# Kernel tuning notes

Hardware: AMD Instinct MI355X
Metric: run time of the kernel (lower is better)

Reference implementation:

```python
import jax, jax.numpy as jnp
import numpy as np
from functools import partial

T, B, IN, H, OUT = 512, 64, 512, 1024, 512


def _qrnn_layer(x, W, b):
    """One QRNN layer (window=1, fo-pool). x: (T,B,D) -> (T,B,H)."""
    g = jnp.einsum('tbd,dh->tbh', x, W) + b        # (T,B,3H)
    z, f, o = jnp.split(g, 3, axis=-1)
    z = jnp.tanh(z)
    f = jax.nn.sigmoid(f)
    o = jax.nn.sigmoid(o)

    def step(c, zf):
        z_t, f_t = zf
        c = f_t * c + (1.0 - f_t) * z_t            # fo-pool recurrence
        return c, c

    c0 = jnp.zeros((x.shape[1], W.shape[1] // 3), x.dtype)
    _, cs = jax.lax.scan(step, c0, (z, f))         # cs: (T,B,H)
    return o * cs


def setup_inputs() -> dict:
    key = jax.random.key(0)
    ks = jax.random.split(key, 5)
    scale = lambda fan_in: 1.0 / np.sqrt(fan_in)
    return {
        'x':   jax.random.normal(ks[0], (T, B, IN), jnp.float32),
        'W0':  jax.random.normal(ks[1], (IN, 3 * H), jnp.float32) * scale(IN),
        'b0':  jnp.zeros((3 * H,), jnp.float32),
        'W1':  jax.random.normal(ks[2], (H, 3 * H), jnp.float32) * scale(H),
        'b1':  jnp.zeros((3 * H,), jnp.float32),
        'Wfc': jax.random.normal(ks[3], (H, OUT), jnp.float32) * scale(H),
        'bfc': jnp.zeros((OUT,), jnp.float32),
    }


def reference(x, W0, b0, W1, b1, Wfc, bfc):
    h = _qrnn_layer(x, W0, b0)                     # layer 0: (T,B,H)
    h = _qrnn_layer(h, W1, b1)                     # layer 1: (T,B,H)
    out = jnp.einsum('tbh,ho->tbo', h, Wfc) + bfc  # fc over all timesteps
    return out
```

## Files before the change

### kernel.cpp

```cpp
#include <hip/hip_runtime.h>
#include <hip/hip_bf16.h>


#define QT 512
#define QB 64
#define QIN 512
#define QH 1024
#define QOUT 512
#define QM (QT * QB)
#define SEG 32
#define SL (QT / SEG)

typedef unsigned short ushort_t;
typedef __attribute__((ext_vector_type(8))) short bf16x8;
typedef __attribute__((ext_vector_type(4))) float f32x4;

__device__ __forceinline__ float u2f(ushort_t u) {
    union { unsigned int i; float f; } v;
    v.i = ((unsigned int)u) << 16;
    return v.f;
}

__device__ __forceinline__ ushort_t f2bf(float f) {
    union { float f; unsigned int i; } v;
    v.f = f;
    unsigned int r = v.i + 0x7fffu + ((v.i >> 16) & 1u);
    return (ushort_t)(r >> 16);
}

__device__ __forceinline__ void glds16(const ushort_t* g, ushort_t* l) {
    __builtin_amdgcn_global_load_lds(
        (const __attribute__((address_space(1))) void*)g,
        (__attribute__((address_space(3))) void*)l, 16, 0, 0);
}

__global__ __launch_bounds__(256) void cvt_bf16(const float* __restrict__ src,
                                                ushort_t* __restrict__ dst) {
    const int i = blockIdx.x * 256 + threadIdx.x;
    float4 v = ((const float4*)src)[i];
    ushort4 o;
    o.x = f2bf(v.x); o.y = f2bf(v.y); o.z = f2bf(v.z); o.w = f2bf(v.w);
    ((ushort4*)dst)[i] = o;
}

__global__ __launch_bounds__(256) void transpose_cvt(
    const float* __restrict__ W, ushort_t* __restrict__ WT, int K, int N) {
    __shared__ float t[32][33];
    const int tx = threadIdx.x & 31, ty = threadIdx.x >> 5;
    const int n0 = blockIdx.x * 32, k0 = blockIdx.y * 32;
#pragma unroll
    for (int i = 0; i < 4; ++i)
        t[ty + 8 * i][tx] = W[(size_t)(k0 + ty + 8 * i) * N + n0 + tx];
    __syncthreads();
#pragma unroll
    for (int i = 0; i < 4; ++i)
        WT[(size_t)(n0 + ty + 8 * i) * K + k0 + tx] = f2bf(t[tx][ty + 8 * i]);
}

template <int MODE, int K>
__global__ __launch_bounds__(512, 2) void gemm256(
    const ushort_t* __restrict__ A, const ushort_t* __restrict__ BT,
    const float* __restrict__ bias, void* __restrict__ out,
    int c0, int CW) {
    constexpr int NT = K / 32;
    __shared__ ushort_t As[4 * 8192];
    __shared__ ushort_t Bs[4 * 8192];

    const int tid = threadIdx.x;
    const int lane = tid & 63;
    const int w = tid >> 6;
    const int wr = w >> 2, wc = w & 3;

    const int gx = gridDim.x;
    const int nwg = gx * gridDim.y;
    int flat = blockIdx.y * gx + blockIdx.x;
    flat = (flat & 7) * (nwg >> 3) + (flat >> 3);
    const int by = flat / gx;
    const int bx = flat - by * gx;
    const int m0 = by * 256;

    int nW, nOut, outstride, gate = 0;
    if (MODE == 0) {
        const int per = CW >> 8;
        gate = bx / per;
        const int nloc = (bx - gate * per) * 256;
        nW = gate * QH + c0 + nloc;
        nOut = gate * CW + nloc;
        outstride = 3 * CW;
    } else {
        nW = bx * 256;
        nOut = nW;
        outstride = QOUT;
    }

    size_t aoff[2], boff[2];
    int ldso[2];
#pragma unroll
    for (int j = 0; j < 2; ++j) {
        const int c = w * 128 + j * 64 + lane;
        const int r = c >> 2;
        const int gs = (c & 3) ^ ((r >> 1) & 3);
        aoff[j] = (size_t)(m0 + r) * K + gs * 8;
        boff[j] = (size_t)(nW + r) * K + gs * 8;
        ldso[j] = w * 1024 + j * 512;
    }

    const int fl = lane & 15, fq = lane >> 4;
    const int laneoff = fl * 32 + ((fq ^ ((fl >> 1) & 3)) << 3);

    f32x4 acc[8][4];
#pragma unroll
    for (int i = 0; i < 8; ++i)
#pragma unroll
        for (int j = 0; j < 4; ++j) acc[i][j] = {0.f, 0.f, 0.f, 0.f};

#pragma unroll
    for (int t = 0; t < 3; ++t) {
        const int slot = t * 8192;
#pragma unroll
        for (int j = 0; j < 2; ++j)
            glds16(A + aoff[j] + t * 32, &As[slot + ldso[j]]);
#pragma unroll
        for (int j = 0; j < 2; ++j)
            glds16(BT + boff[j] + t * 32, &Bs[slot + ldso[j]]);
    }
    asm volatile("s_waitcnt vmcnt(8)" ::: "memory");
    __builtin_amdgcn_s_barrier();

    for (int kt = 0; kt < NT; ++kt) {
        if (kt + 3 < NT) {
            const int slot = ((kt + 3) & 3) * 8192;
            const size_t kb = (size_t)(kt + 3) * 32;
#pragma unroll
            for (int j = 0; j < 2; ++j)
                glds16(A + aoff[j] + kb, &As[slot + ldso[j]]);
#pragma unroll
            for (int j = 0; j < 2; ++j)
                glds16(BT + boff[j] + kb, &Bs[slot + ldso[j]]);
        }
        const int sa = (kt & 3) * 8192 + wr * 4096 + laneoff;
        const int sb = (kt & 3) * 8192 + wc * 2048 + laneoff;
        bf16x8 af[8], bv[4];
#pragma unroll
        for (int i = 0; i < 8; ++i) af[i] = *(const bf16x8*)&As[sa + i * 512];
#pragma unroll
        for (int j = 0; j < 4; ++j) bv[j] = *(const bf16x8*)&Bs[sb + j * 512];
        __builtin_amdgcn_s_setprio(1);
#pragma unroll
        for (int i = 0; i < 8; ++i)
#pragma unroll
            for (int j = 0; j < 4; ++j)
                acc[i][j] = __builtin_amdgcn_mfma_f32_16x16x32_bf16(
                    af[i], bv[j], acc[i][j], 0, 0, 0);
        __builtin_amdgcn_s_setprio(0);
        if (kt < NT - 3)
            asm volatile("s_waitcnt vmcnt(8)" ::: "memory");
        else if (kt == NT - 3)
            asm volatile("s_waitcnt vmcnt(4)" ::: "memory");
        else if (kt == NT - 2)
            asm volatile("s_waitcnt vmcnt(0)" ::: "memory");
        if (kt < NT - 1) __builtin_amdgcn_s_barrier();
    }

    const float ak = (gate == 0) ? 2.8853900817779268f : -1.4426950408889634f;
    const float aa = (gate == 0) ? -2.f : 1.f;
    const float ad = (gate == 0) ? 1.f : 0.f;

#pragma unroll
    for (int j = 0; j < 4; ++j) {
        const int cb = wc * 64 + j * 16 + fl;
        const float bvv = bias[nW + cb];
        const int col = nOut + cb;
#pragma unroll
        for (int i = 0; i < 8; ++i) {
            const int row0 = m0 + wr * 128 + i * 16 + fq * 4;
#pragma unroll
            for (int r = 0; r < 4; ++r) {
                float v = acc[i][j][r] + bvv;
                if (MODE == 0) {
                    v = aa * __builtin_amdgcn_rcpf(
                                 1.f + __builtin_amdgcn_exp2f(ak * v)) +
                        ad;
                    ((ushort_t*)out)[(size_t)(row0 + r) * outstride + col] =
                        f2bf(v);
                } else {
                    ((float*)out)[(size_t)(row0 + r) * outstride + col] = v;
                }
            }
        }
    }
}


__global__ __launch_bounds__(256) void scan_p1(const ushort_t* __restrict__ g,
                                               float* __restrict__ Aseg,
                                               float* __restrict__ Bseg,
                                               int CW) {
    const int idx = blockIdx.x * 256 + threadIdx.x;
    const int hh = idx % CW;
    const int sb = idx / CW;
    const int b = sb % QB;
    const int s = sb / QB;
    const ushort_t* gp = g + ((size_t)(s * SL * QB + b) * 3) * CW + hh;
    const size_t grow = (size_t)QB * 3 * CW;
    float zv[SL], fv[SL];
#pragma unroll
    for (int t = 0; t < SL; ++t) {
        zv[t] = u2f(gp[0]);
        fv[t] = u2f(gp[CW]);
        gp += grow;
    }
    float A = 1.f, Bc = 0.f;
#pragma unroll
    for (int t = 0; t < SL; ++t) {
        Bc = fv[t] * Bc + (1.f - fv[t]) * zv[t];
        A *= fv[t];
    }
    Aseg[idx] = A;
    Bseg[idx] = Bc;
}

__global__ __launch_bounds__(256) void scan_p2(const float* __restrict__ Aseg,
                                               const float* __restrict__ Bseg,
                                               float* __restrict__ cstart,
                                               int CW) {
    const int idx = blockIdx.x * 256 + threadIdx.x;
    const size_t stride = (size_t)QB * CW;
    float Av[SEG], Bv[SEG];
#pragma unroll
    for (int s = 0; s < SEG; ++s) {
        Av[s] = Aseg[s * stride + idx];
        Bv[s] = Bseg[s * stride + idx];
    }
    float c = 0.f;
#pragma unroll
    for (int s = 0; s < SEG; ++s) {
        cstart[s * stride + idx] = c;
        c = Av[s] * c + Bv[s];
    }
}

__global__ __launch_bounds__(256) void scan_p3(const ushort_t* __restrict__ g,
                                               const float* __restrict__ cstart,
                                               ushort_t* __restrict__ h,
                                               int c0, int CW) {
    const int idx = blockIdx.x * 256 + threadIdx.x;
    const int hh = idx % CW;
    const int sb = idx / CW;
    const int b = sb % QB;
    const int s = sb / QB;
    const ushort_t* gp = g + ((size_t)(s * SL * QB + b) * 3) * CW + hh;
    ushort_t* hp = h + (size_t)(s * SL * QB + b) * QH + c0 + hh;
    const size_t grow = (size_t)QB * 3 * CW;
    const size_t hrow = (size_t)QB * QH;
    float zv[SL], fv[SL], ov[SL];
#pragma unroll
    for (int t = 0; t < SL; ++t) {
        zv[t] = u2f(gp[0]);
        fv[t] = u2f(gp[CW]);
        ov[t] = u2f(gp[2 * CW]);
        gp += grow;
    }
    float c = cstart[idx];
#pragma unroll
    for (int t = 0; t < SL; ++t) {
        c = fv[t] * c + (1.f - fv[t]) * zv[t];
        *hp = f2bf(ov[t] * c);
        hp += hrow;
    }
}

extern "C" void kernel_launch(void* const* d_in, const int* in_sizes, int n_in,
                              void* d_out, int out_size, void* d_ws,
                              size_t ws_size, hipStream_t stream) {
    const float* x   = (const float*)d_in[0];
    const float* W0  = (const float*)d_in[1];
    const float* b0  = (const float*)d_in[2];
    const float* W1  = (const float*)d_in[3];
    const float* b1  = (const float*)d_in[4];
    const float* Wfc = (const float*)d_in[5];
    const float* bfc = (const float*)d_in[6];
    float* out = (float*)d_out;

    char* p = (char*)d_ws;
    ushort_t* h0   = (ushort_t*)p;  p += (size_t)QM * QH * 2;
    ushort_t* h1   = (ushort_t*)p;
    ushort_t* x_bf = (ushort_t*)p;  p += (size_t)QM * QH * 2;
    ushort_t* W0T  = (ushort_t*)p;  p += (size_t)3 * QH * QIN * 2;
    ushort_t* W1T  = (ushort_t*)p;  p += (size_t)3 * QH * QH * 2;
    ushort_t* WfcT = (ushort_t*)p;  p += (size_t)QOUT * QH * 2;
    const size_t base = (size_t)(p - (char*)d_ws);

    int CW = QH;
    while (CW > 256 &&
           base + 3 * (size_t)QB * CW * SEG * 4 + (size_t)QM * 3 * CW * 2 >
               ws_size)
        CW >>= 1;
    const int nch = QH / CW;

    float* Aseg   = (float*)p;  p += (size_t)QB * CW * SEG * 4;
    float* Bseg   = (float*)p;  p += (size_t)QB * CW * SEG * 4;
    float* cstart = (float*)p;  p += (size_t)QB * CW * SEG * 4;
    ushort_t* g   = (ushort_t*)p;

    dim3 blk(256);
    dim3 blk5(512);

    cvt_bf16<<<dim3(QM * QIN / 1024), blk, 0, stream>>>(x, x_bf);
    transpose_cvt<<<dim3(3 * QH / 32, QIN / 32), blk, 0, stream>>>(
        W0, W0T, QIN, 3 * QH);
    transpose_cvt<<<dim3(3 * QH / 32, QH / 32), blk, 0, stream>>>(
        W1, W1T, QH, 3 * QH);
    transpose_cvt<<<dim3(QOUT / 32, QH / 32), blk, 0, stream>>>(
        Wfc, WfcT, QH, QOUT);

    const dim3 ggrid(3 * (CW >> 8), QM / 256);
    const dim3 p13grid(SEG * QB * CW / 256);
    const dim3 p2grid(QB * CW / 256);

    for (int ci = 0; ci < nch; ++ci) {
        gemm256<0, QIN><<<ggrid, blk5, 0, stream>>>(x_bf, W0T, b0, g,
                                                    ci * CW, CW);
        scan_p1<<<p13grid, blk, 0, stream>>>(g, Aseg, Bseg, CW);
        scan_p2<<<p2grid, blk, 0, stream>>>(Aseg, Bseg, cstart, CW);
        scan_p3<<<p13grid, blk, 0, stream>>>(g, cstart, h0, ci * CW, CW);
    }
    for (int ci = 0; ci < nch; ++ci) {
        gemm256<0, QH><<<ggrid, blk5, 0, stream>>>(h0, W1T, b1, g,
                                                   ci * CW, CW);
        scan_p1<<<p13grid, blk, 0, stream>>>(g, Aseg, Bseg, CW);
        scan_p2<<<p2grid, blk, 0, stream>>>(Aseg, Bseg, cstart, CW);
        scan_p3<<<p13grid, blk, 0, stream>>>(g, cstart, h1, ci * CW, CW);
    }
    gemm256<1, QH><<<dim3(QOUT / 256, QM / 256), blk5, 0, stream>>>(
        h1, WfcT, bfc, out, 0, 0);
}
```

Before: 786.1 us.

## Split GEMM K-step into two half-tile phases with interleaved LDS reads and prefetch

The main GEMM loop now splits each K-tile into two phases. The first half of the A fragments is loaded and multiplied while the A-tile prefetch is issued, then the second half is loaded alongside the B-tile prefetch. Extra workgroup barriers and sched_barrier fences enforce the ordering so LDS reads, global-to-LDS copies and MFMAs from different waves interleave, and register pressure from fragments drops. The epilogue loop order is also changed to iterate rows outer and columns inner, with bias hoisted. The cost is three extra barriers per K iteration.

```diff
diff --git a/kernel.cpp b/kernel.cpp
--- a/kernel.cpp
+++ b/kernel.cpp
@@ -128,30 +128,56 @@
     __builtin_amdgcn_s_barrier();
 
     for (int kt = 0; kt < NT; ++kt) {
-        if (kt + 3 < NT) {
-            const int slot = ((kt + 3) & 3) * 8192;
-            const size_t kb = (size_t)(kt + 3) * 32;
+        const int slot = (kt & 3) * 8192;
+        const int sa = slot + wr * 4096 + laneoff;
+        const int sb = slot + wc * 2048 + laneoff;
+        const bool pf = (kt + 3 < NT);
+        const int pslot = ((kt + 3) & 3) * 8192;
+        const size_t kb = (size_t)(kt + 3) * 32;
+
+        bf16x8 a0[4], a1[4], bv[4];
+#pragma unroll
+        for (int i = 0; i < 4; ++i) a0[i] = *(const bf16x8*)&As[sa + i * 512];
+#pragma unroll
+        for (int j = 0; j < 4; ++j) bv[j] = *(const bf16x8*)&Bs[sb + j * 512];
+        if (pf) {
 #pragma unroll
             for (int j = 0; j < 2; ++j)
-                glds16(A + aoff[j] + kb, &As[slot + ldso[j]]);
-#pragma unroll
-            for (int j = 0; j < 2; ++j)
-                glds16(BT + boff[j] + kb, &Bs[slot + ldso[j]]);
+                glds16(A + aoff[j] + kb, &As[pslot + ldso[j]]);
         }
-        const int sa = (kt & 3) * 8192 + wr * 4096 + laneoff;
-        const int sb = (kt & 3) * 8192 + wc * 2048 + laneoff;
-        bf16x8 af[8], bv[4];
-#pragma unroll
-        for (int i = 0; i < 8; ++i) af[i] = *(const bf16x8*)&As[sa + i * 512];
-#pragma unroll
-        for (int j = 0; j < 4; ++j) bv[j] = *(const bf16x8*)&Bs[sb + j * 512];
+        __builtin_amdgcn_sched_barrier(0);
+        __builtin_amdgcn_s_barrier();
+        asm volatile("s_waitcnt lgkmcnt(0)" ::: "memory");
+        __builtin_amdgcn_sched_barrier(0);
         __builtin_amdgcn_s_setprio(1);
 #pragma unroll
-        for (int i = 0; i < 8; ++i)
+        for (int i = 0; i < 4; ++i)
 #pragma unroll
             for (int j = 0; j < 4; ++j)
                 acc[i][j] = __builtin_amdgcn_mfma_f32_16x16x32_bf16(
-                    af[i], bv[j], acc[i][j], 0, 0, 0);
+                    a0[i], bv[j], acc[i][j], 0, 0, 0);
+        __builtin_amdgcn_s_setprio(0);
+        __builtin_amdgcn_sched_barrier(0);
+        __builtin_amdgcn_s_barrier();
+#pragma unroll
+        for (int i = 0; i < 4; ++i)
+            a1[i] = *(const bf16x8*)&As[sa + (4 + i) * 512];
+        if (pf) {
+#pragma unroll
+            for (int j = 0; j < 2; ++j)
+                glds16(BT + boff[j] + kb, &Bs[pslot + ldso[j]]);
+        }
+        __builtin_amdgcn_sched_barrier(0);
+        __builtin_amdgcn_s_barrier();
+        asm volatile("s_waitcnt lgkmcnt(0)" ::: "memory");
+        __builtin_amdgcn_sched_barrier(0);
+        __builtin_amdgcn_s_setprio(1);
+#pragma unroll
+        for (int i = 0; i < 4; ++i)
+#pragma unroll
+            for (int j = 0; j < 4; ++j)
+                acc[4 + i][j] = __builtin_amdgcn_mfma_f32_16x16x32_bf16(
+                    a1[i], bv[j], acc[4 + i][j], 0, 0, 0);
         __builtin_amdgcn_s_setprio(0);
         if (kt < NT - 3)
             asm volatile("s_waitcnt vmcnt(8)" ::: "memory");
@@ -159,6 +185,7 @@
             asm volatile("s_waitcnt vmcnt(4)" ::: "memory");
         else if (kt == NT - 2)
             asm volatile("s_waitcnt vmcnt(0)" ::: "memory");
+        __builtin_amdgcn_sched_barrier(0);
         if (kt < NT - 1) __builtin_amdgcn_s_barrier();
     }
 
@@ -166,25 +193,25 @@
     const float aa = (gate == 0) ? -2.f : 1.f;
     const float ad = (gate == 0) ? 1.f : 0.f;
 
-#pragma unroll
-    for (int j = 0; j < 4; ++j) {
-        const int cb = wc * 64 + j * 16 + fl;
-        const float bvv = bias[nW + cb];
-        const int col = nOut + cb;
-#pragma unroll
-        for (int i = 0; i < 8; ++i) {
-            const int row0 = m0 + wr * 128 + i * 16 + fq * 4;
-#pragma unroll
-            for (int r = 0; r < 4; ++r) {
-                float v = acc[i][j][r] + bvv;
+    float bvv[4];
+#pragma unroll
+    for (int j = 0; j < 4; ++j) bvv[j] = bias[nW + wc * 64 + j * 16 + fl];
+#pragma unroll
+    for (int i = 0; i < 8; ++i) {
+#pragma unroll
+        for (int r = 0; r < 4; ++r) {
+            const int row = m0 + wr * 128 + i * 16 + fq * 4 + r;
+#pragma unroll
+            for (int j = 0; j < 4; ++j) {
+                const int col = nOut + wc * 64 + j * 16 + fl;
+                float v = acc[i][j][r] + bvv[j];
                 if (MODE == 0) {
                     v = aa * __builtin_amdgcn_rcpf(
                                  1.f + __builtin_amdgcn_exp2f(ak * v)) +
                         ad;
-                    ((ushort_t*)out)[(size_t)(row0 + r) * outstride + col] =
-                        f2bf(v);
+                    ((ushort_t*)out)[(size_t)row * outstride + col] = f2bf(v);
                 } else {
-                    ((float*)out)[(size_t)(row0 + r) * outstride + col] = v;
+                    ((float*)out)[(size_t)row * outstride + col] = v;
                 }
             }
         }
```

Measured after the change: 674.8 us. 14.2% less time.
